# Performance work log

Measured on AMD Instinct MI355X. Metric: run time of the kernel, lower is better.

Reference implementation:

```python
import jax, jax.numpy as jnp
import numpy as np

B, T, C = 64, 256, 384
H, HD = 6, 64


def setup_inputs() -> dict:
    key = jax.random.key(0)
    ks = jax.random.split(key, 6)
    x = jax.random.normal(ks[0], (B, T, C), dtype=jnp.float32)
    s = 1.0 / np.sqrt(C)
    Wq = jax.random.normal(ks[1], (H, C, HD), dtype=jnp.float32) * s
    Wk = jax.random.normal(ks[2], (H, C, HD), dtype=jnp.float32) * s
    Wv = jax.random.normal(ks[3], (H, C, HD), dtype=jnp.float32) * s
    Wp = jax.random.normal(ks[4], (C, C), dtype=jnp.float32) * s
    bp = jnp.zeros((C,), dtype=jnp.float32)
    return {"x": x, "Wq": Wq, "Wk": Wk, "Wv": Wv, "Wp": Wp, "bp": bp}


def reference(x, Wq, Wk, Wv, Wp, bp):
    # per-head projections (no bias), vectorized over heads
    q = jnp.einsum('btc,hcd->bhtd', x, Wq)
    k = jnp.einsum('btc,hcd->bhtd', x, Wk)
    v = jnp.einsum('btc,hcd->bhtd', x, Wv)
    scale = HD ** (-0.5)
    scores = jnp.einsum('bhtd,bhsd->bhts', q, k) * scale  # [B,H,T,T]
    causal = jnp.tril(jnp.ones((T, T), dtype=bool))
    scores = jnp.where(causal, scores, -jnp.inf)
    wei = jax.nn.softmax(scores, axis=-1)  # dropout is identity in eval mode
    out = jnp.einsum('bhts,bhsd->bhtd', wei, v)
    out = out.transpose(0, 2, 1, 3).reshape(B, T, C)  # concat heads
    return out @ Wp.T + bp
```

## Files before the change

### kernel.cpp

```cpp
#include <hip/hip_runtime.h>
#include <hip/hip_bf16.h>
#include <cstdint>
#include <cstddef>

#define B_ 64
#define T_ 256
#define C_ 384
#define H_ 6
#define HD_ 64

using u16 = unsigned short;
typedef __attribute__((ext_vector_type(8))) short short8;
typedef __attribute__((ext_vector_type(4))) short short4_;
typedef __attribute__((ext_vector_type(4))) float f32x4;

__device__ __forceinline__ u16 f2bf(float f) {
    union { float f; uint32_t u; } x{f};
    uint32_t r = x.u + 0x7fffu + ((x.u >> 16) & 1u);
    return (u16)(r >> 16);
}

__global__ void k_prep(const float* __restrict__ x, const float* __restrict__ Wq,
                       const float* __restrict__ Wk, const float* __restrict__ Wv,
                       const float* __restrict__ Wp, u16* __restrict__ xb,
                       u16* __restrict__ wqkv, u16* __restrict__ wpb) {
    int bid = blockIdx.x;
    if (bid < 3072) {
        int i = (bid * 256 + threadIdx.x) * 8;
        const f32x4* p = (const f32x4*)(x + i);
        f32x4 a = p[0], b = p[1];
        short8 s;
        s[0] = (short)f2bf(a[0]); s[1] = (short)f2bf(a[1]);
        s[2] = (short)f2bf(a[2]); s[3] = (short)f2bf(a[3]);
        s[4] = (short)f2bf(b[0]); s[5] = (short)f2bf(b[1]);
        s[6] = (short)f2bf(b[2]); s[7] = (short)f2bf(b[3]);
        *(short8*)(xb + i) = s;
    } else if (bid < 3180) {
        __shared__ u16 Tt[64 * 65];
        int pb = bid - 3072;
        int which = pb / 36, rem = pb % 36;
        int h = rem / 6, cc0 = (rem % 6) * 64;
        const float* W = (which == 0) ? Wq : ((which == 1) ? Wk : Wv);
        int d = threadIdx.x & 63, cr0 = threadIdx.x >> 6;
#pragma unroll
        for (int p = 0; p < 16; ++p) {
            int cr = p * 4 + cr0;
            Tt[cr * 65 + d] = f2bf(W[(h * 384 + cc0 + cr) * 64 + d]);
        }
        __syncthreads();
        int ccl = threadIdx.x & 63, dl0 = threadIdx.x >> 6;
        int nbase = which * 384 + h * 64;
#pragma unroll
        for (int p = 0; p < 16; ++p) {
            int dl = p * 4 + dl0;
            wqkv[(size_t)(nbase + dl) * 384 + cc0 + ccl] = Tt[ccl * 65 + dl];
        }
    } else {
        int i = ((bid - 3180) * 256 + threadIdx.x) * 8;
        const f32x4* p = (const f32x4*)(Wp + i);
        f32x4 a = p[0], b = p[1];
        short8 s;
        s[0] = (short)f2bf(a[0]); s[1] = (short)f2bf(a[1]);
        s[2] = (short)f2bf(a[2]); s[3] = (short)f2bf(a[3]);
        s[4] = (short)f2bf(b[0]); s[5] = (short)f2bf(b[1]);
        s[6] = (short)f2bf(b[2]); s[7] = (short)f2bf(b[3]);
        *(short8*)(wpb + i) = s;
    }
}

template<int NROWS>
__device__ __forceinline__ void stage_rows(const u16* __restrict__ gbase, int ld,
                                           u16* lds_tile, int wid, int lane, int k0) {
#pragma unroll
    for (int i = 0; i < NROWS / 32; ++i) {
        int chunk = wid * (NROWS / 32) + i;
        int row = chunk * 8 + (lane >> 3);
        int pslot = lane & 7;
        const u16* gp = gbase + (size_t)row * ld + k0 + ((pslot ^ (row & 7)) << 3);
        u16* lp = lds_tile + chunk * 512;
        __builtin_amdgcn_global_load_lds((const __attribute__((address_space(1))) void*)gp,
                                         (__attribute__((address_space(3))) void*)lp, 16, 0, 0);
    }
}

__device__ __forceinline__ void stage_tile(const u16* __restrict__ gbase, int ld,
                                           u16* lds_tile, int wid, int lane, int k0) {
    stage_rows<128>(gbase, ld, lds_tile, wid, lane, k0);
}

__device__ __forceinline__ short8 read_frag(const u16* lds_tile, int row, int ks, int g) {
    int pslot = (ks * 4 + g) ^ (row & 7);
    return *(const short8*)&lds_tile[row * 64 + pslot * 8];
}

#define GEMM_PIPE_LOOP(NT)                                                        \
    int cur = 0;                                                                  \
    for (int t = 0; t < (NT); ++t) {                                              \
        if (t < (NT) - 1) {                                                       \
            stage_tile(Ag, 384, &lds[cur ^ 1][0], wid, lane, (t + 1) * 64);       \
            stage_tile(Bg, 384, &lds[cur ^ 1][8192], wid, lane, (t + 1) * 64);    \
            asm volatile("s_waitcnt vmcnt(8)" ::: "memory");                      \
        } else {                                                                  \
            asm volatile("s_waitcnt vmcnt(0)" ::: "memory");                      \
        }                                                                         \
        __builtin_amdgcn_s_barrier();                                             \
        __builtin_amdgcn_sched_barrier(0);                                        \
        const u16* A = &lds[cur][0];                                              \
        const u16* Bm = &lds[cur][8192];                                          \
        short8 af[2][4], bf[2][4];                                                \
        _Pragma("unroll")                                                         \
        for (int ks = 0; ks < 2; ++ks) {                                          \
            _Pragma("unroll")                                                     \
            for (int mf = 0; mf < 4; ++mf) af[ks][mf] = read_frag(A, wm * 64 + mf * 16 + c, ks, g); \
            _Pragma("unroll")                                                     \
            for (int nf = 0; nf < 4; ++nf) bf[ks][nf] = read_frag(Bm, wn * 64 + nf * 16 + c, ks, g); \
        }                                                                         \
        _Pragma("unroll")                                                         \
        for (int ks = 0; ks < 2; ++ks)                                            \
            _Pragma("unroll")                                                     \
            for (int mf = 0; mf < 4; ++mf)                                        \
                _Pragma("unroll")                                                 \
                for (int nf = 0; nf < 4; ++nf)                                    \
                    acc[mf][nf] = __builtin_amdgcn_mfma_f32_16x16x32_bf16(af[ks][mf], bf[ks][nf], acc[mf][nf], 0, 0, 0); \
        __builtin_amdgcn_sched_barrier(0);                                        \
        __builtin_amdgcn_s_barrier();                                             \
        cur ^= 1;                                                                 \
    }

__global__ __launch_bounds__(256, 2) void k_gemm_qkv(const u16* __restrict__ xb, const u16* __restrict__ wb,
                                                     u16* __restrict__ q, u16* __restrict__ k,
                                                     u16* __restrict__ v) {
    __shared__ alignas(16) u16 lds[2][16384];
    const int tid = threadIdx.x, lane = tid & 63, wid = tid >> 6;
    const int wm = wid >> 1, wn = wid & 1, g = lane >> 4, c = lane & 15;
    const int n0 = blockIdx.x * 128, m0 = blockIdx.y * 128;
    const u16* Ag = xb + (size_t)m0 * 384;
    const u16* Bg = wb + (size_t)n0 * 384;
    f32x4 acc[4][4] = {};
    stage_tile(Ag, 384, &lds[0][0], wid, lane, 0);
    stage_tile(Bg, 384, &lds[0][8192], wid, lane, 0);
    GEMM_PIPE_LOOP(6)
    const int which = n0 / 384;
    u16* dst = (which == 0) ? q : ((which == 1) ? k : v);
    const int h = ((n0 + wn * 64) % 384) / 64;
#pragma unroll
    for (int mf = 0; mf < 4; ++mf)
#pragma unroll
        for (int nf = 0; nf < 4; ++nf)
#pragma unroll
            for (int r = 0; r < 4; ++r) {
                int m = m0 + wm * 64 + mf * 16 + g * 4 + r;
                int d = nf * 16 + c;
                int b = m >> 8, t = m & 255;
                dst[((b * H_ + h) * T_ + t) * HD_ + d] = f2bf(acc[mf][nf][r]);
            }
}

__global__ __launch_bounds__(256, 2) void k_attn(const u16* __restrict__ q, const u16* __restrict__ k,
                                                 const u16* __restrict__ v, u16* __restrict__ ao) {
    __shared__ alignas(16) u16 Kl[2][64 * 64];
    __shared__ alignas(16) u16 Vt[2][64][72];
    const int tid = threadIdx.x, bh = blockIdx.x;
    const int lane = tid & 63, wid = tid >> 6;
    const int g = lane >> 4, c = lane & 15;
    const int bq = bh * 256;

    const int vd0 = (tid & 15) * 4;
    const int vs0 = (tid >> 4) * 4;
    const int kb0 = ((vs0 >> 5) << 5) | (((vs0 >> 2) & 3) << 3) | (((vs0 >> 4) & 1) << 2);

    short8 qB[4][2];
#pragma unroll
    for (int qf = 0; qf < 4; ++qf)
#pragma unroll
        for (int ks = 0; ks < 2; ++ks) {
            int t = wid * 64 + qf * 16 + c;
            qB[qf][ks] = *(const short8*)&q[(bq + t) * 64 + ks * 32 + g * 8];
        }
    float mrun[4], lrun[4];
#pragma unroll
    for (int i = 0; i < 4; ++i) { mrun[i] = -1e30f; lrun[i] = 0.f; }
    f32x4 o[4][4] = {};

    short4_ vv[4];
    stage_rows<64>(k + (size_t)(bq) * 64, 64, &Kl[0][0], wid, lane, 0);
#pragma unroll
    for (int i = 0; i < 4; ++i)
        vv[i] = *(const short4_*)&v[(size_t)(bq + vs0 + i) * 64 + vd0];
#pragma unroll
    for (int j = 0; j < 4; ++j) {
        short4_ w4;
#pragma unroll
        for (int i = 0; i < 4; ++i) w4[i] = vv[i][j];
        *(short4_*)&Vt[0][vd0 + j][kb0] = w4;
    }
    __syncthreads();

    int buf = 0;
    for (int kt = 0; kt < 4; ++kt) {
        if (kt < 3) {
            stage_rows<64>(k + (size_t)(bq + (kt + 1) * 64) * 64, 64, &Kl[buf ^ 1][0], wid, lane, 0);
#pragma unroll
            for (int i = 0; i < 4; ++i)
                vv[i] = *(const short4_*)&v[(size_t)(bq + (kt + 1) * 64 + vs0 + i) * 64 + vd0];
        }
        if (kt <= wid) {
            f32x4 st[4][4] = {};
            __builtin_amdgcn_s_setprio(1);
#pragma unroll
            for (int ks = 0; ks < 2; ++ks) {
                short8 kA[4];
#pragma unroll
                for (int sf = 0; sf < 4; ++sf)
                    kA[sf] = read_frag(&Kl[buf][0], sf * 16 + c, ks, g);
#pragma unroll
                for (int sf = 0; sf < 4; ++sf)
#pragma unroll
                    for (int qf = 0; qf < 4; ++qf)
                        st[sf][qf] = __builtin_amdgcn_mfma_f32_16x16x32_bf16(kA[sf], qB[qf][ks], st[sf][qf], 0, 0, 0);
            }
            __builtin_amdgcn_s_setprio(0);
            float pm[4] = {-1e30f, -1e30f, -1e30f, -1e30f};
#pragma unroll
            for (int sf = 0; sf < 4; ++sf)
#pragma unroll
                for (int qf = 0; qf < 4; ++qf)
#pragma unroll
                    for (int r = 0; r < 4; ++r) {
                        float val = st[sf][qf][r] * 0.125f;
                        if (kt == wid) {
                            int s_loc = sf * 16 + g * 4 + r, q_loc = qf * 16 + c;
                            if (s_loc > q_loc) val = -1e30f;
                        }
                        st[sf][qf][r] = val;
                        pm[qf] = fmaxf(pm[qf], val);
                    }
            float alpha[4];
#pragma unroll
            for (int qf = 0; qf < 4; ++qf) {
                pm[qf] = fmaxf(pm[qf], __shfl_xor(pm[qf], 16));
                pm[qf] = fmaxf(pm[qf], __shfl_xor(pm[qf], 32));
                float mnew = fmaxf(mrun[qf], pm[qf]);
                alpha[qf] = __expf(mrun[qf] - mnew);
                mrun[qf] = mnew;
            }
            short8 pA[4][2];
#pragma unroll
            for (int qf = 0; qf < 4; ++qf) {
                float ls = 0.f;
#pragma unroll
                for (int ks = 0; ks < 2; ++ks) {
                    short8 pa;
#pragma unroll
                    for (int half = 0; half < 2; ++half) {
                        f32x4 sv = st[2 * ks + half][qf];
#pragma unroll
                        for (int r = 0; r < 4; ++r) {
                            float p = __expf(sv[r] - mrun[qf]);
                            ls += p;
                            pa[half * 4 + r] = (short)f2bf(p);
                        }
                    }
                    pA[qf][ks] = pa;
                }
                ls += __shfl_xor(ls, 16);
                ls += __shfl_xor(ls, 32);
                lrun[qf] = lrun[qf] * alpha[qf] + ls;
            }
#pragma unroll
            for (int mf = 0; mf < 4; ++mf)
#pragma unroll
                for (int r = 0; r < 4; ++r) {
                    float aof = __shfl(alpha[mf], g * 4 + r);
#pragma unroll
                    for (int df = 0; df < 4; ++df)
                        o[mf][df][r] *= aof;
                }
            __builtin_amdgcn_s_setprio(1);
#pragma unroll
            for (int ks = 0; ks < 2; ++ks) {
                short8 vB[4];
#pragma unroll
                for (int df = 0; df < 4; ++df)
                    vB[df] = *(short8*)&Vt[buf][df * 16 + c][ks * 32 + g * 8];
#pragma unroll
                for (int mf = 0; mf < 4; ++mf)
#pragma unroll
                    for (int df = 0; df < 4; ++df)
                        o[mf][df] = __builtin_amdgcn_mfma_f32_16x16x32_bf16(pA[mf][ks], vB[df], o[mf][df], 0, 0, 0);
            }
            __builtin_amdgcn_s_setprio(0);
        }
        if (kt < 3) {
#pragma unroll
            for (int j = 0; j < 4; ++j) {
                short4_ w4;
#pragma unroll
                for (int i = 0; i < 4; ++i) w4[i] = vv[i][j];
                *(short4_*)&Vt[buf ^ 1][vd0 + j][kb0] = w4;
            }
        }
        __syncthreads();
        buf ^= 1;
    }
    const int bb = bh / H_, hh = bh % H_;
#pragma unroll
    for (int mf = 0; mf < 4; ++mf)
#pragma unroll
        for (int r = 0; r < 4; ++r) {
            float inv = 1.0f / __shfl(lrun[mf], g * 4 + r);
            int t = wid * 64 + mf * 16 + g * 4 + r;
#pragma unroll
            for (int df = 0; df < 4; ++df) {
                int d = df * 16 + c;
                ao[((size_t)(bb * T_ + t)) * C_ + hh * 64 + d] = f2bf(o[mf][df][r] * inv);
            }
        }
}

__global__ __launch_bounds__(256, 2) void k_gemm_proj(const u16* __restrict__ ab, const u16* __restrict__ wp,
                                                      const float* __restrict__ bp, float* __restrict__ out) {
    __shared__ alignas(16) u16 lds[2][16384];
    const int tid = threadIdx.x, lane = tid & 63, wid = tid >> 6;
    const int wm = wid >> 1, wn = wid & 1, g = lane >> 4, c = lane & 15;
    const int n0 = blockIdx.x * 128, m0 = blockIdx.y * 128;
    const u16* Ag = ab + (size_t)m0 * 384;
    const u16* Bg = wp + (size_t)n0 * 384;
    f32x4 acc[4][4] = {};
    stage_tile(Ag, 384, &lds[0][0], wid, lane, 0);
    stage_tile(Bg, 384, &lds[0][8192], wid, lane, 0);
    GEMM_PIPE_LOOP(6)
#pragma unroll
    for (int mf = 0; mf < 4; ++mf)
#pragma unroll
        for (int nf = 0; nf < 4; ++nf)
#pragma unroll
            for (int r = 0; r < 4; ++r) {
                int m = m0 + wm * 64 + mf * 16 + g * 4 + r;
                int n = n0 + wn * 64 + nf * 16 + c;
                out[(size_t)m * C_ + n] = acc[mf][nf][r] + bp[n];
            }
}


extern "C" void kernel_launch(void* const* d_in, const int* in_sizes, int n_in,
                              void* d_out, int out_size, void* d_ws, size_t ws_size,
                              hipStream_t stream) {
    const float* x  = (const float*)d_in[0];
    const float* Wq = (const float*)d_in[1];
    const float* Wk = (const float*)d_in[2];
    const float* Wv = (const float*)d_in[3];
    const float* Wp = (const float*)d_in[4];
    const float* bp = (const float*)d_in[5];
    float* out = (float*)d_out;

    char* ws = (char*)d_ws;
    u16* xb   = (u16*)(ws);
    u16* wqkv = (u16*)(ws + 12582912);
    u16* wpb  = (u16*)(ws + 13467648);
    u16* qb   = (u16*)(ws + 13762560);
    u16* kb   = (u16*)(ws + 26345472);
    u16* vb   = (u16*)(ws + 38928384);
    u16* ab   = (u16*)(ws + 51511296);

    k_prep<<<3252, 256, 0, stream>>>(x, Wq, Wk, Wv, Wp, xb, wqkv, wpb);
    k_gemm_qkv<<<dim3(9, 128), 256, 0, stream>>>(xb, wqkv, qb, kb, vb);
    k_attn<<<384, 256, 0, stream>>>(qb, kb, vb, ab);
    k_gemm_proj<<<dim3(3, 128), 256, 0, stream>>>(ab, wpb, bp, out);
}
```

Measured before the change: 73.52 us.

## Fuse x fp32-to-bf16 conversion into QKV GEMM A-tile loading

The separate conversion pass that wrote a bf16 copy of x to workspace is removed. The QKV GEMM now loads fp32 x directly into registers, converts it to bf16 and writes it into swizzled LDS, with a register-prefetch double buffer that replaces async global-to-LDS loads for A. This avoids a 12 MB bf16 write and re-read. In exchange, x is re-read as fp32 (twice the bytes) by each of the 9 column blocks, and the conversion ALU work now sits inside the GEMM loop. The attention kernel is only moved in the file, and the workspace offsets shift.

Result: slower. 100.2 us (+36.3%).

```diff
diff --git a/kernel.cpp b/kernel.cpp
--- a/kernel.cpp
+++ b/kernel.cpp
@@ -20,25 +20,13 @@
     return (u16)(r >> 16);
 }
 
-__global__ void k_prep(const float* __restrict__ x, const float* __restrict__ Wq,
-                       const float* __restrict__ Wk, const float* __restrict__ Wv,
-                       const float* __restrict__ Wp, u16* __restrict__ xb,
-                       u16* __restrict__ wqkv, u16* __restrict__ wpb) {
+__global__ void k_prep_w(const float* __restrict__ Wq, const float* __restrict__ Wk,
+                         const float* __restrict__ Wv, const float* __restrict__ Wp,
+                         u16* __restrict__ wqkv, u16* __restrict__ wpb) {
     int bid = blockIdx.x;
-    if (bid < 3072) {
-        int i = (bid * 256 + threadIdx.x) * 8;
-        const f32x4* p = (const f32x4*)(x + i);
-        f32x4 a = p[0], b = p[1];
-        short8 s;
-        s[0] = (short)f2bf(a[0]); s[1] = (short)f2bf(a[1]);
-        s[2] = (short)f2bf(a[2]); s[3] = (short)f2bf(a[3]);
-        s[4] = (short)f2bf(b[0]); s[5] = (short)f2bf(b[1]);
-        s[6] = (short)f2bf(b[2]); s[7] = (short)f2bf(b[3]);
-        *(short8*)(xb + i) = s;
-    } else if (bid < 3180) {
+    if (bid < 108) {
         __shared__ u16 Tt[64 * 65];
-        int pb = bid - 3072;
-        int which = pb / 36, rem = pb % 36;
+        int which = bid / 36, rem = bid % 36;
         int h = rem / 6, cc0 = (rem % 6) * 64;
         const float* W = (which == 0) ? Wq : ((which == 1) ? Wk : Wv);
         int d = threadIdx.x & 63, cr0 = threadIdx.x >> 6;
@@ -56,7 +44,7 @@
             wqkv[(size_t)(nbase + dl) * 384 + cc0 + ccl] = Tt[ccl * 65 + dl];
         }
     } else {
-        int i = ((bid - 3180) * 256 + threadIdx.x) * 8;
+        int i = ((bid - 108) * 256 + threadIdx.x) * 8;
         const f32x4* p = (const f32x4*)(Wp + i);
         f32x4 a = p[0], b = p[1];
         short8 s;
@@ -91,6 +79,241 @@
 __device__ __forceinline__ short8 read_frag(const u16* lds_tile, int row, int ks, int g) {
     int pslot = (ks * 4 + g) ^ (row & 7);
     return *(const short8*)&lds_tile[row * 64 + pslot * 8];
+}
+
+__device__ __forceinline__ void write_A(u16* tile, int row, int half, const f32x4* a) {
+#pragma unroll
+    for (int j = 0; j < 4; ++j) {
+        short8 s;
+#pragma unroll
+        for (int e = 0; e < 8; ++e) s[e] = (short)f2bf(a[j * 2 + (e >> 2)][e & 3]);
+        int slot = half * 4 + j;
+        *(short8*)&tile[row * 64 + ((slot ^ (row & 7)) << 3)] = s;
+    }
+}
+
+__global__ __launch_bounds__(256, 2) void k_gemm_qkv(const float* __restrict__ x, const u16* __restrict__ wb,
+                                                     u16* __restrict__ q, u16* __restrict__ k,
+                                                     u16* __restrict__ v) {
+    __shared__ alignas(16) u16 lds[2][16384];
+    const int tid = threadIdx.x, lane = tid & 63, wid = tid >> 6;
+    const int wm = wid >> 1, wn = wid & 1, g = lane >> 4, c = lane & 15;
+    const int n0 = blockIdx.x * 128, m0 = blockIdx.y * 128;
+    const float* Ag = x + (size_t)m0 * 384;
+    const u16* Bg = wb + (size_t)n0 * 384;
+    const int arow = tid >> 1, ahalf = tid & 1;
+    const float* arp = Ag + (size_t)arow * 384 + ahalf * 32;
+    f32x4 acc[4][4] = {};
+    f32x4 areg[8];
+#pragma unroll
+    for (int i = 0; i < 8; ++i) areg[i] = *(const f32x4*)&arp[i * 4];
+    stage_rows<128>(Bg, 384, &lds[0][8192], wid, lane, 0);
+    write_A(&lds[0][0], arow, ahalf, areg);
+    __syncthreads();
+    int cur = 0;
+    for (int t = 0; t < 6; ++t) {
+        if (t < 5) {
+#pragma unroll
+            for (int i = 0; i < 8; ++i) areg[i] = *(const f32x4*)&arp[(t + 1) * 64 + i * 4];
+            stage_rows<128>(Bg, 384, &lds[cur ^ 1][8192], wid, lane, (t + 1) * 64);
+        }
+        const u16* A = &lds[cur][0];
+        const u16* Bm = &lds[cur][8192];
+        short8 af[2][4], bf[2][4];
+#pragma unroll
+        for (int ks = 0; ks < 2; ++ks) {
+#pragma unroll
+            for (int mf = 0; mf < 4; ++mf) af[ks][mf] = read_frag(A, wm * 64 + mf * 16 + c, ks, g);
+#pragma unroll
+            for (int nf = 0; nf < 4; ++nf) bf[ks][nf] = read_frag(Bm, wn * 64 + nf * 16 + c, ks, g);
+        }
+#pragma unroll
+        for (int ks = 0; ks < 2; ++ks)
+#pragma unroll
+            for (int mf = 0; mf < 4; ++mf)
+#pragma unroll
+                for (int nf = 0; nf < 4; ++nf)
+                    acc[mf][nf] = __builtin_amdgcn_mfma_f32_16x16x32_bf16(af[ks][mf], bf[ks][nf], acc[mf][nf], 0, 0, 0);
+        if (t < 5) write_A(&lds[cur ^ 1][0], arow, ahalf, areg);
+        __syncthreads();
+        cur ^= 1;
+    }
+    const int which = n0 / 384;
+    u16* dst = (which == 0) ? q : ((which == 1) ? k : v);
+    const int h = ((n0 + wn * 64) % 384) / 64;
+#pragma unroll
+    for (int mf = 0; mf < 4; ++mf)
+#pragma unroll
+        for (int nf = 0; nf < 4; ++nf)
+#pragma unroll
+            for (int r = 0; r < 4; ++r) {
+                int m = m0 + wm * 64 + mf * 16 + g * 4 + r;
+                int d = nf * 16 + c;
+                int b = m >> 8, t = m & 255;
+                dst[((b * H_ + h) * T_ + t) * HD_ + d] = f2bf(acc[mf][nf][r]);
+            }
+}
+
+__global__ __launch_bounds__(256, 2) void k_attn(const u16* __restrict__ q, const u16* __restrict__ k,
+                                                 const u16* __restrict__ v, u16* __restrict__ ao) {
+    __shared__ alignas(16) u16 Kl[2][64 * 64];
+    __shared__ alignas(16) u16 Vt[2][64][72];
+    const int tid = threadIdx.x, bh = blockIdx.x;
+    const int lane = tid & 63, wid = tid >> 6;
+    const int g = lane >> 4, c = lane & 15;
+    const int bq = bh * 256;
+
+    const int vd0 = (tid & 15) * 4;
+    const int vs0 = (tid >> 4) * 4;
+    const int kb0 = ((vs0 >> 5) << 5) | (((vs0 >> 2) & 3) << 3) | (((vs0 >> 4) & 1) << 2);
+
+    short8 qB[4][2];
+#pragma unroll
+    for (int qf = 0; qf < 4; ++qf)
+#pragma unroll
+        for (int ks = 0; ks < 2; ++ks) {
+            int t = wid * 64 + qf * 16 + c;
+            qB[qf][ks] = *(const short8*)&q[(bq + t) * 64 + ks * 32 + g * 8];
+        }
+    float mrun[4], lrun[4];
+#pragma unroll
+    for (int i = 0; i < 4; ++i) { mrun[i] = -1e30f; lrun[i] = 0.f; }
+    f32x4 o[4][4] = {};
+
+    short4_ vv[4];
+    stage_rows<64>(k + (size_t)(bq) * 64, 64, &Kl[0][0], wid, lane, 0);
+#pragma unroll
+    for (int i = 0; i < 4; ++i)
+        vv[i] = *(const short4_*)&v[(size_t)(bq + vs0 + i) * 64 + vd0];
+#pragma unroll
+    for (int j = 0; j < 4; ++j) {
+        short4_ w4;
+#pragma unroll
+        for (int i = 0; i < 4; ++i) w4[i] = vv[i][j];
+        *(short4_*)&Vt[0][vd0 + j][kb0] = w4;
+    }
+    __syncthreads();
+
+    int buf = 0;
+    for (int kt = 0; kt < 4; ++kt) {
+        if (kt < 3) {
+            stage_rows<64>(k + (size_t)(bq + (kt + 1) * 64) * 64, 64, &Kl[buf ^ 1][0], wid, lane, 0);
+#pragma unroll
+            for (int i = 0; i < 4; ++i)
+                vv[i] = *(const short4_*)&v[(size_t)(bq + (kt + 1) * 64 + vs0 + i) * 64 + vd0];
+        }
+        if (kt <= wid) {
+            f32x4 st[4][4] = {};
+            __builtin_amdgcn_s_setprio(1);
+#pragma unroll
+            for (int ks = 0; ks < 2; ++ks) {
+                short8 kA[4];
+#pragma unroll
+                for (int sf = 0; sf < 4; ++sf)
+                    kA[sf] = read_frag(&Kl[buf][0], sf * 16 + c, ks, g);
+#pragma unroll
+                for (int sf = 0; sf < 4; ++sf)
+#pragma unroll
+                    for (int qf = 0; qf < 4; ++qf)
+                        st[sf][qf] = __builtin_amdgcn_mfma_f32_16x16x32_bf16(kA[sf], qB[qf][ks], st[sf][qf], 0, 0, 0);
+            }
+            __builtin_amdgcn_s_setprio(0);
+            float pm[4] = {-1e30f, -1e30f, -1e30f, -1e30f};
+#pragma unroll
+            for (int sf = 0; sf < 4; ++sf)
+#pragma unroll
+                for (int qf = 0; qf < 4; ++qf)
+#pragma unroll
+                    for (int r = 0; r < 4; ++r) {
+                        float val = st[sf][qf][r] * 0.125f;
+                        if (kt == wid) {
+                            int s_loc = sf * 16 + g * 4 + r, q_loc = qf * 16 + c;
+                            if (s_loc > q_loc) val = -1e30f;
+                        }
+                        st[sf][qf][r] = val;
+                        pm[qf] = fmaxf(pm[qf], val);
+                    }
+            float alpha[4];
+#pragma unroll
+            for (int qf = 0; qf < 4; ++qf) {
+                pm[qf] = fmaxf(pm[qf], __shfl_xor(pm[qf], 16));
+                pm[qf] = fmaxf(pm[qf], __shfl_xor(pm[qf], 32));
+                float mnew = fmaxf(mrun[qf], pm[qf]);
+                alpha[qf] = __expf(mrun[qf] - mnew);
+                mrun[qf] = mnew;
+            }
+            short8 pA[4][2];
+#pragma unroll
+            for (int qf = 0; qf < 4; ++qf) {
+                float ls = 0.f;
+#pragma unroll
+                for (int ks = 0; ks < 2; ++ks) {
+                    short8 pa;
+#pragma unroll
+                    for (int half = 0; half < 2; ++half) {
+                        f32x4 sv = st[2 * ks + half][qf];
+#pragma unroll
+                        for (int r = 0; r < 4; ++r) {
+                            float p = __expf(sv[r] - mrun[qf]);
+                            ls += p;
+                            pa[half * 4 + r] = (short)f2bf(p);
+                        }
+                    }
+                    pA[qf][ks] = pa;
+                }
+                ls += __shfl_xor(ls, 16);
+                ls += __shfl_xor(ls, 32);
+                lrun[qf] = lrun[qf] * alpha[qf] + ls;
+            }
+#pragma unroll
+            for (int mf = 0; mf < 4; ++mf)
+#pragma unroll
+                for (int r = 0; r < 4; ++r) {
+                    float aof = __shfl(alpha[mf], g * 4 + r);
+#pragma unroll
+                    for (int df = 0; df < 4; ++df)
+                        o[mf][df][r] *= aof;
+                }
+            __builtin_amdgcn_s_setprio(1);
+#pragma unroll
+            for (int ks = 0; ks < 2; ++ks) {
+                short8 vB[4];
+#pragma unroll
+                for (int df = 0; df < 4; ++df)
+                    vB[df] = *(short8*)&Vt[buf][df * 16 + c][ks * 32 + g * 8];
+#pragma unroll
+                for (int mf = 0; mf < 4; ++mf)
+#pragma unroll
+                    for (int df = 0; df < 4; ++df)
+                        o[mf][df] = __builtin_amdgcn_mfma_f32_16x16x32_bf16(pA[mf][ks], vB[df], o[mf][df], 0, 0, 0);
+            }
+            __builtin_amdgcn_s_setprio(0);
+        }
+        if (kt < 3) {
+#pragma unroll
+            for (int j = 0; j < 4; ++j) {
+                short4_ w4;
+#pragma unroll
+                for (int i = 0; i < 4; ++i) w4[i] = vv[i][j];
+                *(short4_*)&Vt[buf ^ 1][vd0 + j][kb0] = w4;
+            }
+        }
+        __syncthreads();
+        buf ^= 1;
+    }
+    const int bb = bh / H_, hh = bh % H_;
+#pragma unroll
+    for (int mf = 0; mf < 4; ++mf)
+#pragma unroll
+        for (int r = 0; r < 4; ++r) {
+            float inv = 1.0f / __shfl(lrun[mf], g * 4 + r);
+            int t = wid * 64 + mf * 16 + g * 4 + r;
+#pragma unroll
+            for (int df = 0; df < 4; ++df) {
+                int d = df * 16 + c;
+                ao[((size_t)(bb * T_ + t)) * C_ + hh * 64 + d] = f2bf(o[mf][df][r] * inv);
+            }
+        }
 }
 
 #define GEMM_PIPE_LOOP(NT)                                                        \
@@ -127,197 +350,6 @@
         cur ^= 1;                                                                 \
     }
 
-__global__ __launch_bounds__(256, 2) void k_gemm_qkv(const u16* __restrict__ xb, const u16* __restrict__ wb,
-                                                     u16* __restrict__ q, u16* __restrict__ k,
-                                                     u16* __restrict__ v) {
-    __shared__ alignas(16) u16 lds[2][16384];
-    const int tid = threadIdx.x, lane = tid & 63, wid = tid >> 6;
-    const int wm = wid >> 1, wn = wid & 1, g = lane >> 4, c = lane & 15;
-    const int n0 = blockIdx.x * 128, m0 = blockIdx.y * 128;
-    const u16* Ag = xb + (size_t)m0 * 384;
-    const u16* Bg = wb + (size_t)n0 * 384;
-    f32x4 acc[4][4] = {};
-    stage_tile(Ag, 384, &lds[0][0], wid, lane, 0);
-    stage_tile(Bg, 384, &lds[0][8192], wid, lane, 0);
-    GEMM_PIPE_LOOP(6)
-    const int which = n0 / 384;
-    u16* dst = (which == 0) ? q : ((which == 1) ? k : v);
-    const int h = ((n0 + wn * 64) % 384) / 64;
-#pragma unroll
-    for (int mf = 0; mf < 4; ++mf)
-#pragma unroll
-        for (int nf = 0; nf < 4; ++nf)
-#pragma unroll
-            for (int r = 0; r < 4; ++r) {
-                int m = m0 + wm * 64 + mf * 16 + g * 4 + r;
-                int d = nf * 16 + c;
-                int b = m >> 8, t = m & 255;
-                dst[((b * H_ + h) * T_ + t) * HD_ + d] = f2bf(acc[mf][nf][r]);
-            }
-}
-
-__global__ __launch_bounds__(256, 2) void k_attn(const u16* __restrict__ q, const u16* __restrict__ k,
-                                                 const u16* __restrict__ v, u16* __restrict__ ao) {
-    __shared__ alignas(16) u16 Kl[2][64 * 64];
-    __shared__ alignas(16) u16 Vt[2][64][72];
-    const int tid = threadIdx.x, bh = blockIdx.x;
-    const int lane = tid & 63, wid = tid >> 6;
-    const int g = lane >> 4, c = lane & 15;
-    const int bq = bh * 256;
-
-    const int vd0 = (tid & 15) * 4;
-    const int vs0 = (tid >> 4) * 4;
-    const int kb0 = ((vs0 >> 5) << 5) | (((vs0 >> 2) & 3) << 3) | (((vs0 >> 4) & 1) << 2);
-
-    short8 qB[4][2];
-#pragma unroll
-    for (int qf = 0; qf < 4; ++qf)
-#pragma unroll
-        for (int ks = 0; ks < 2; ++ks) {
-            int t = wid * 64 + qf * 16 + c;
-            qB[qf][ks] = *(const short8*)&q[(bq + t) * 64 + ks * 32 + g * 8];
-        }
-    float mrun[4], lrun[4];
-#pragma unroll
-    for (int i = 0; i < 4; ++i) { mrun[i] = -1e30f; lrun[i] = 0.f; }
-    f32x4 o[4][4] = {};
-
-    short4_ vv[4];
-    stage_rows<64>(k + (size_t)(bq) * 64, 64, &Kl[0][0], wid, lane, 0);
-#pragma unroll
-    for (int i = 0; i < 4; ++i)
-        vv[i] = *(const short4_*)&v[(size_t)(bq + vs0 + i) * 64 + vd0];
-#pragma unroll
-    for (int j = 0; j < 4; ++j) {
-        short4_ w4;
-#pragma unroll
-        for (int i = 0; i < 4; ++i) w4[i] = vv[i][j];
-        *(short4_*)&Vt[0][vd0 + j][kb0] = w4;
-    }
-    __syncthreads();
-
-    int buf = 0;
-    for (int kt = 0; kt < 4; ++kt) {
-        if (kt < 3) {
-            stage_rows<64>(k + (size_t)(bq + (kt + 1) * 64) * 64, 64, &Kl[buf ^ 1][0], wid, lane, 0);
-#pragma unroll
-            for (int i = 0; i < 4; ++i)
-                vv[i] = *(const short4_*)&v[(size_t)(bq + (kt + 1) * 64 + vs0 + i) * 64 + vd0];
-        }
-        if (kt <= wid) {
-            f32x4 st[4][4] = {};
-            __builtin_amdgcn_s_setprio(1);
-#pragma unroll
-            for (int ks = 0; ks < 2; ++ks) {
-                short8 kA[4];
-#pragma unroll
-                for (int sf = 0; sf < 4; ++sf)
-                    kA[sf] = read_frag(&Kl[buf][0], sf * 16 + c, ks, g);
-#pragma unroll
-                for (int sf = 0; sf < 4; ++sf)
-#pragma unroll
-                    for (int qf = 0; qf < 4; ++qf)
-                        st[sf][qf] = __builtin_amdgcn_mfma_f32_16x16x32_bf16(kA[sf], qB[qf][ks], st[sf][qf], 0, 0, 0);
-            }
-            __builtin_amdgcn_s_setprio(0);
-            float pm[4] = {-1e30f, -1e30f, -1e30f, -1e30f};
-#pragma unroll
-            for (int sf = 0; sf < 4; ++sf)
-#pragma unroll
-                for (int qf = 0; qf < 4; ++qf)
-#pragma unroll
-                    for (int r = 0; r < 4; ++r) {
-                        float val = st[sf][qf][r] * 0.125f;
-                        if (kt == wid) {
-                            int s_loc = sf * 16 + g * 4 + r, q_loc = qf * 16 + c;
-                            if (s_loc > q_loc) val = -1e30f;
-                        }
-                        st[sf][qf][r] = val;
-                        pm[qf] = fmaxf(pm[qf], val);
-                    }
-            float alpha[4];
-#pragma unroll
-            for (int qf = 0; qf < 4; ++qf) {
-                pm[qf] = fmaxf(pm[qf], __shfl_xor(pm[qf], 16));
-                pm[qf] = fmaxf(pm[qf], __shfl_xor(pm[qf], 32));
-                float mnew = fmaxf(mrun[qf], pm[qf]);
-                alpha[qf] = __expf(mrun[qf] - mnew);
-                mrun[qf] = mnew;
-            }
-            short8 pA[4][2];
-#pragma unroll
-            for (int qf = 0; qf < 4; ++qf) {
-                float ls = 0.f;
-#pragma unroll
-                for (int ks = 0; ks < 2; ++ks) {
-                    short8 pa;
-#pragma unroll
-                    for (int half = 0; half < 2; ++half) {
-                        f32x4 sv = st[2 * ks + half][qf];
-#pragma unroll
-                        for (int r = 0; r < 4; ++r) {
-                            float p = __expf(sv[r] - mrun[qf]);
-                            ls += p;
-                            pa[half * 4 + r] = (short)f2bf(p);
-                        }
-                    }
-                    pA[qf][ks] = pa;
-                }
-                ls += __shfl_xor(ls, 16);
-                ls += __shfl_xor(ls, 32);
-                lrun[qf] = lrun[qf] * alpha[qf] + ls;
-            }
-#pragma unroll
-            for (int mf = 0; mf < 4; ++mf)
-#pragma unroll
-                for (int r = 0; r < 4; ++r) {
-                    float aof = __shfl(alpha[mf], g * 4 + r);
-#pragma unroll
-                    for (int df = 0; df < 4; ++df)
-                        o[mf][df][r] *= aof;
-                }
-            __builtin_amdgcn_s_setprio(1);
-#pragma unroll
-            for (int ks = 0; ks < 2; ++ks) {
-                short8 vB[4];
-#pragma unroll
-                for (int df = 0; df < 4; ++df)
-                    vB[df] = *(short8*)&Vt[buf][df * 16 + c][ks * 32 + g * 8];
-#pragma unroll
-                for (int mf = 0; mf < 4; ++mf)
-#pragma unroll
-                    for (int df = 0; df < 4; ++df)
-                        o[mf][df] = __builtin_amdgcn_mfma_f32_16x16x32_bf16(pA[mf][ks], vB[df], o[mf][df], 0, 0, 0);
-            }
-            __builtin_amdgcn_s_setprio(0);
-        }
-        if (kt < 3) {
-#pragma unroll
-            for (int j = 0; j < 4; ++j) {
-                short4_ w4;
-#pragma unroll
-                for (int i = 0; i < 4; ++i) w4[i] = vv[i][j];
-                *(short4_*)&Vt[buf ^ 1][vd0 + j][kb0] = w4;
-            }
-        }
-        __syncthreads();
-        buf ^= 1;
-    }
-    const int bb = bh / H_, hh = bh % H_;
-#pragma unroll
-    for (int mf = 0; mf < 4; ++mf)
-#pragma unroll
-        for (int r = 0; r < 4; ++r) {
-            float inv = 1.0f / __shfl(lrun[mf], g * 4 + r);
-            int t = wid * 64 + mf * 16 + g * 4 + r;
-#pragma unroll
-            for (int df = 0; df < 4; ++df) {
-                int d = df * 16 + c;
-                ao[((size_t)(bb * T_ + t)) * C_ + hh * 64 + d] = f2bf(o[mf][df][r] * inv);
-            }
-        }
-}
-
 __global__ __launch_bounds__(256, 2) void k_gemm_proj(const u16* __restrict__ ab, const u16* __restrict__ wp,
                                                       const float* __restrict__ bp, float* __restrict__ out) {
     __shared__ alignas(16) u16 lds[2][16384];
@@ -355,16 +387,15 @@
     float* out = (float*)d_out;
 
     char* ws = (char*)d_ws;
-    u16* xb   = (u16*)(ws);
-    u16* wqkv = (u16*)(ws + 12582912);
-    u16* wpb  = (u16*)(ws + 13467648);
-    u16* qb   = (u16*)(ws + 13762560);
-    u16* kb   = (u16*)(ws + 26345472);
-    u16* vb   = (u16*)(ws + 38928384);
-    u16* ab   = (u16*)(ws + 51511296);
-
-    k_prep<<<3252, 256, 0, stream>>>(x, Wq, Wk, Wv, Wp, xb, wqkv, wpb);
-    k_gemm_qkv<<<dim3(9, 128), 256, 0, stream>>>(xb, wqkv, qb, kb, vb);
+    u16* wqkv = (u16*)(ws);
+    u16* wpb  = (u16*)(ws + 884736);
+    u16* qb   = (u16*)(ws + 1179648);
+    u16* kb   = (u16*)(ws + 13762560);
+    u16* vb   = (u16*)(ws + 26345472);
+    u16* ab   = (u16*)(ws + 38928384);
+
+    k_prep_w<<<180, 256, 0, stream>>>(Wq, Wk, Wv, Wp, wqkv, wpb);
+    k_gemm_qkv<<<dim3(9, 128), 256, 0, stream>>>(x, wqkv, qb, kb, vb);
     k_attn<<<384, 256, 0, stream>>>(qb, kb, vb, ab);
     k_gemm_proj<<<dim3(3, 128), 256, 0, stream>>>(ab, wpb, bp, out);
 }
```
